# Performance work log

Hardware: AMD Instinct MI355X
Metric: run time of the kernel (lower is better)

The kernel has to match this reference:

```python
import jax, jax.numpy as jnp
import numpy as np
import math

BLUR_K = [1.0, 3.0, 3.0, 1.0]
EPS = 1e-8


def _make_blur_kernel(upsample_factor=2):
    k = jnp.asarray(BLUR_K, dtype=jnp.float32)
    k = k[None, :] * k[:, None]
    k = k / k.sum()
    return k * (upsample_factor ** 2)


def setup_inputs() -> dict:
    key = jax.random.key(0)
    ks = jax.random.split(key, 5)
    B, Cin, Cout, K, S, H, W = 16, 256, 128, 3, 512, 64, 64
    x = jax.random.normal(ks[0], (B, Cin, H, W), dtype=jnp.float32)
    style = jax.random.normal(ks[1], (B, S), dtype=jnp.float32)
    weight = jax.random.normal(ks[2], (1, Cout, Cin, K, K), dtype=jnp.float32)
    mod_w = jax.random.normal(ks[3], (Cin, S), dtype=jnp.float32) * (1.0 / math.sqrt(S))
    mod_b = jnp.ones((Cin,), dtype=jnp.float32)  # StyleGAN2 modulation bias init = 1
    return {"x": x, "style": style, "weight": weight, "mod_w": mod_w, "mod_b": mod_b}


def reference(x, style, weight, mod_w, mod_b):
    B, Cin, H, W = x.shape
    Cout = weight.shape[1]
    K = weight.shape[-1]
    scale = 1.0 / math.sqrt(Cin * K * K)

    # modulation: Linear(style_dim -> in_channel)
    s = style @ mod_w.T + mod_b                      # (B, Cin)
    w = scale * weight * s[:, None, :, None, None]   # (B, Cout, Cin, K, K)
    demod = jax.lax.rsqrt(jnp.sum(w * w, axis=(2, 3, 4)) + EPS)  # (B, Cout)
    w = w * demod[:, :, None, None, None]

    # per-sample conv_transpose2d(stride=2, padding=0, groups=B)
    # == lhs-dilated grouped correlation with spatially-flipped kernel
    kernel = jnp.flip(w, axis=(3, 4)).reshape(B * Cout, Cin, K, K)
    xg = x.reshape(1, B * Cin, H, W)
    out = jax.lax.conv_general_dilated(
        xg, kernel,
        window_strides=(1, 1),
        padding=((K - 1, K - 1), (K - 1, K - 1)),
        lhs_dilation=(2, 2),
        feature_group_count=B,
        dimension_numbers=("NCHW", "OIHW", "NCHW"),
    )  # (1, B*Cout, 2H+K-2, 2W+K-2) -> here (1, B*Cout, 2H+1, 2W+1)
    Ht, Wt = out.shape[2], out.shape[3]

    # Blur2 / upfirdn2d(up=1, down=1, pad=(pad0, pad1))
    # p = len(blur_kernel) - 2 - (K - 1); pad0 = (p+1)//2 + 1; pad1 = p//2 + 1
    p = len(BLUR_K) - 2 - (K - 1)
    pad0 = (p + 1) // 2 + 1
    pad1 = p // 2 + 1
    bk = _make_blur_kernel()                       # (4, 4)
    bw = jnp.flip(bk, axis=(0, 1))[None, None]     # (1, 1, 4, 4)
    outs = out.reshape(B * Cout, 1, Ht, Wt)
    blurred = jax.lax.conv_general_dilated(
        outs, bw,
        window_strides=(1, 1),
        padding=((pad0, pad1), (pad0, pad1)),
        dimension_numbers=("NCHW", "OIHW", "NCHW"),
    )
    Hb, Wb = blurred.shape[2], blurred.shape[3]
    return blurred.reshape(B, Cout, Hb, Wb)
```

## Files before the change

kernel.cpp:

```cpp
#include <hip/hip_runtime.h>
#include <stdint.h>

#define CIN 256
#define COUT 128
#define SDIM 512
#define NB 16

#define XP_RSTRIDE 16896
#define XP_BSTRIDE 1115136
#define A_BSTRIDE (512*2304)

typedef __attribute__((ext_vector_type(8))) short short8;
typedef __attribute__((ext_vector_type(4))) float f32x4;

__device__ __forceinline__ float bf2f(unsigned short h) {
  union { unsigned int u; float f; } v; v.u = ((unsigned int)h) << 16; return v.f;
}
__device__ __forceinline__ unsigned short f2bf(float f) {
  union { float f; unsigned int u; } v; v.f = f;
  return (unsigned short)((v.u + 0x7fffu + ((v.u >> 16) & 1u)) >> 16);
}
__device__ __forceinline__ void gll16(const void* g, void* l) {
  __builtin_amdgcn_global_load_lds(
      (const __attribute__((address_space(1))) unsigned int*)g,
      (__attribute__((address_space(3))) unsigned int*)l, 16, 0, 0);
}

__global__ __launch_bounds__(256) void k_detect(
    const unsigned short* __restrict__ xr, int* __restrict__ flag) {
  __shared__ int red[4];
  int t = threadIdx.x, cnt = 0;
  for (int i = t; i < 8192; i += 256) {
    int e = (xr[2*i] >> 7) & 0xff;
    cnt += (e > 90 && e < 145) ? 1 : 0;
  }
  #pragma unroll
  for (int off = 32; off > 0; off >>= 1) cnt += __shfl_down(cnt, off);
  if ((t & 63) == 0) red[t >> 6] = cnt;
  __syncthreads();
  if (t == 0) *flag = (red[0] + red[1] + red[2] + red[3] < 5000) ? 1 : 0;
}

__global__ __launch_bounds__(256) void k_style(
    const void* __restrict__ style_v, const void* __restrict__ mod_w_v,
    const void* __restrict__ mod_b_v, const int* __restrict__ flag,
    float* __restrict__ s_out) {
  __shared__ float st[SDIM];
  int b = blockIdx.x, t = threadIdx.x;
  int isf = *flag;
  float acc;
  if (!isf) {
    const unsigned short* style = (const unsigned short*)style_v;
    const unsigned short* mod_w = (const unsigned short*)mod_w_v;
    const unsigned short* mod_b = (const unsigned short*)mod_b_v;
    st[t]       = bf2f(style[b*SDIM + t]);
    st[t + 256] = bf2f(style[b*SDIM + t + 256]);
    __syncthreads();
    const uint4* wr = (const uint4*)(mod_w + (size_t)t*SDIM);
    acc = bf2f(mod_b[t]);
    #pragma unroll 4
    for (int s8 = 0; s8 < SDIM/8; ++s8) {
      uint4 p = wr[s8];
      int sb = s8*8;
      acc += bf2f((unsigned short)(p.x & 0xffff))*st[sb]
           + bf2f((unsigned short)(p.x >> 16))   *st[sb+1]
           + bf2f((unsigned short)(p.y & 0xffff))*st[sb+2]
           + bf2f((unsigned short)(p.y >> 16))   *st[sb+3]
           + bf2f((unsigned short)(p.z & 0xffff))*st[sb+4]
           + bf2f((unsigned short)(p.z >> 16))   *st[sb+5]
           + bf2f((unsigned short)(p.w & 0xffff))*st[sb+6]
           + bf2f((unsigned short)(p.w >> 16))   *st[sb+7];
    }
  } else {
    const float* style = (const float*)style_v;
    const float* mod_w = (const float*)mod_w_v;
    const float* mod_b = (const float*)mod_b_v;
    st[t]       = style[b*SDIM + t];
    st[t + 256] = style[b*SDIM + t + 256];
    __syncthreads();
    const float4* wr = (const float4*)(mod_w + (size_t)t*SDIM);
    acc = mod_b[t];
    #pragma unroll 4
    for (int s4 = 0; s4 < SDIM/4; ++s4) {
      float4 p = wr[s4];
      int sb = s4*4;
      acc += p.x*st[sb] + p.y*st[sb+1] + p.z*st[sb+2] + p.w*st[sb+3];
    }
  }
  s_out[b*CIN + t] = acc;
}

__global__ __launch_bounds__(256) void k_weights(
    const void* __restrict__ weight_v,
    const float* __restrict__ s_in,
    const int* __restrict__ flag,
    unsigned short* __restrict__ Aw) {
  int co = blockIdx.x, b = blockIdx.y, ci = threadIdx.x;
  int isf = *flag;
  float sm = 0.0208333333333333f * s_in[b*CIN + ci];
  float w9[9]; float ss = 0.f;
  if (!isf) {
    const unsigned short* wp = (const unsigned short*)weight_v + ((size_t)co*CIN + ci)*9;
    #pragma unroll
    for (int k = 0; k < 9; ++k) { float v = bf2f(wp[k]) * sm; w9[k] = v; ss += v*v; }
  } else {
    const float* wp = (const float*)weight_v + ((size_t)co*CIN + ci)*9;
    #pragma unroll
    for (int k = 0; k < 9; ++k) { float v = wp[k] * sm; w9[k] = v; ss += v*v; }
  }
  #pragma unroll
  for (int off = 32; off > 0; off >>= 1) ss += __shfl_down(ss, off);
  __shared__ float red[4];
  if ((ci & 63) == 0) red[ci >> 6] = ss;
  __syncthreads();
  float demod = rsqrtf(red[0] + red[1] + red[2] + red[3] + 1e-8f);
  #pragma unroll
  for (int k = 0; k < 9; ++k) w9[k] *= demod;
  const float F[4] = {0.25f, 0.75f, 0.75f, 0.25f};
  float C6[6][6];
  #pragma unroll
  for (int ty = 0; ty < 6; ++ty) {
    #pragma unroll
    for (int tx = 0; tx < 6; ++tx) {
      float acc = 0.f;
      #pragma unroll
      for (int ay = 0; ay < 3; ++ay) {
        int fy = ay - ty + 3;
        if (fy < 0 || fy > 3) continue;
        float ra = 0.f;
        #pragma unroll
        for (int ax = 0; ax < 3; ++ax) {
          int fx = ax - tx + 3;
          if (fx < 0 || fx > 3) continue;
          ra += w9[ay*3 + ax] * F[fx];
        }
        acc += ra * F[fy];
      }
      C6[ty][tx] = acc;
    }
  }
  unsigned short* Ab = Aw + (size_t)b*A_BSTRIDE;
  #pragma unroll
  for (int py = 0; py < 2; ++py) {
    #pragma unroll
    for (int px = 0; px < 2; ++px) {
      unsigned short* Am = Ab + (size_t)(py*256 + co*2 + px)*2304 + ci;
      #pragma unroll
      for (int dh = -1; dh <= 1; ++dh) {
        #pragma unroll
        for (int dw = -1; dw <= 1; ++dw) {
          int tap = (dh+1)*3 + (dw+1);
          Am[tap*256] = f2bf(C6[py - 2*dh + 2][px - 2*dw + 2]);
        }
      }
    }
  }
}

__global__ __launch_bounds__(256) void k_transpose(
    const void* __restrict__ x_v,
    const int* __restrict__ flag,
    unsigned short* __restrict__ xp) {
  int r_out = blockIdx.x, b = blockIdx.y, t = threadIdx.x;
  unsigned short* rp = xp + (size_t)b*XP_BSTRIDE + (size_t)r_out*XP_RSTRIDE;
  int r_in = r_out - 1;
  if (r_in < 0 || r_in >= 64) {
    uint4 z = make_uint4(0,0,0,0);
    #pragma unroll
    for (int i = 0; i < 9; ++i) {
      int idx = i*256 + t;
      if (idx < 2112) ((uint4*)rp)[idx] = z;
    }
    return;
  }
  if (t < 64) {
    uint4 z = make_uint4(0,0,0,0);
    int col = (t < 32) ? 0 : 65;
    ((uint4*)(rp + col*256))[t & 31] = z;
  }
  int isf = *flag;
  __shared__ unsigned int lds32[64*33];
  int tci = t >> 3;
  int tc8 = t & 7;
  int cS  = t >> 2;
  int jg  = t & 3;
  for (int g4 = 0; g4 < 4; ++g4) {
    int ci0 = g4 * 64;
    int ci = ci0 + tci*2;
    size_t base = (((size_t)b*CIN + ci)*64 + r_in)*64 + tc8*8;
    unsigned int v[8];
    if (isf) {
      const float* s0 = (const float*)x_v + base;
      const float* s1 = s0 + 4096;
      float4 a0 = ((const float4*)s0)[0], a1 = ((const float4*)s0)[1];
      float4 b0 = ((const float4*)s1)[0], b1 = ((const float4*)s1)[1];
      v[0] = f2bf(a0.x) | ((unsigned int)f2bf(b0.x) << 16);
      v[1] = f2bf(a0.y) | ((unsigned int)f2bf(b0.y) << 16);
      v[2] = f2bf(a0.z) | ((unsigned int)f2bf(b0.z) << 16);
      v[3] = f2bf(a0.w) | ((unsigned int)f2bf(b0.w) << 16);
      v[4] = f2bf(a1.x) | ((unsigned int)f2bf(b1.x) << 16);
      v[5] = f2bf(a1.y) | ((unsigned int)f2bf(b1.y) << 16);
      v[6] = f2bf(a1.z) | ((unsigned int)f2bf(b1.z) << 16);
      v[7] = f2bf(a1.w) | ((unsigned int)f2bf(b1.w) << 16);
    } else {
      const unsigned short* s0 = (const unsigned short*)x_v + base;
      const unsigned short* s1 = s0 + 4096;
      union { uint4 q; unsigned short h[8]; } u0, u1;
      u0.q = *(const uint4*)s0; u1.q = *(const uint4*)s1;
      #pragma unroll
      for (int j = 0; j < 8; ++j)
        v[j] = (unsigned int)u0.h[j] | ((unsigned int)u1.h[j] << 16);
    }
    if (g4) __syncthreads();
    #pragma unroll
    for (int j = 0; j < 8; ++j)
      lds32[(tc8*8 + j)*33 + tci] = v[j];
    __syncthreads();
    union { unsigned int o[8]; uint4 q[2]; } ob;
    #pragma unroll
    for (int w = 0; w < 8; ++w)
      ob.o[w] = lds32[cS*33 + jg*8 + w];
    uint4* dst = (uint4*)(rp + (size_t)(cS+1)*256 + ci0 + jg*16);
    dst[0] = ob.q[0];
    dst[1] = ob.q[1];
  }
}

__global__ __launch_bounds__(256) void k_gemm(
    const unsigned short* __restrict__ Aw,
    const unsigned short* __restrict__ xp,
    const int* __restrict__ flag,
    void* __restrict__ out) {
  __shared__ __align__(16) unsigned short As[128*32];
  __shared__ __align__(16) unsigned short Bs[128*32];
  int g = blockIdx.x;
  int b  = ((g & 7) << 1) | ((g >> 3) & 1);
  int mt = (g >> 4) & 3;
  int nt = g >> 6;
  int yy0 = nt << 1;
  int t = threadIdx.x;
  int wave = t >> 6, lane = t & 63;
  int row = t >> 2, part = t & 3;
  int isf = *flag;

  int partS = part ^ ((row >> 2) & 3);
  const unsigned short* pA0 = Aw + (size_t)b*A_BSTRIDE + (size_t)(mt*128 + row)*2304 + partS*8;
  const unsigned short* pA1 = pA0 + (size_t)64*2304;
  const unsigned short* pB0 = xp + (size_t)b*XP_BSTRIDE + (size_t)(yy0 + 1)*XP_RSTRIDE
                              + (size_t)(row + 1)*256 + partS*8;
  const unsigned short* pB1 = pB0 + XP_RSTRIDE;
  unsigned short* lA0 = &As[row*32 + part*8];
  unsigned short* lA1 = &As[(row + 64)*32 + part*8];
  unsigned short* lB0 = &Bs[row*32 + part*8];
  unsigned short* lB1 = &Bs[(row + 64)*32 + part*8];

  f32x4 acc[4][4];
  #pragma unroll
  for (int i = 0; i < 4; ++i)
    #pragma unroll
    for (int j = 0; j < 4; ++j)
      acc[i][j] = (f32x4){0.f, 0.f, 0.f, 0.f};

  int mb = (wave >> 1) << 6;
  int nb = (wave & 1) << 6;
  int l15 = lane & 15, q = lane >> 4;
  int qs = q ^ ((l15 >> 2) & 3);

  for (int tap = 0; tap < 9; ++tap) {
    int dh = (tap >= 6) ? 1 : ((tap >= 3) ? 0 : -1);
    int dwx = tap - (dh + 1)*3 - 1;
    const unsigned short* a0 = pA0 + tap*256;
    const unsigned short* a1 = pA1 + tap*256;
    const unsigned short* b0 = pB0 + dh*XP_RSTRIDE + dwx*256;
    const unsigned short* b1 = b0 + XP_RSTRIDE;
    #pragma unroll
    for (int kk = 0; kk < 8; ++kk) {
      gll16(a0 + kk*32, lA0);
      gll16(a1 + kk*32, lA1);
      gll16(b0 + kk*32, lB0);
      gll16(b1 + kk*32, lB1);
      __syncthreads();
      short8 af[4], bfv[4];
      #pragma unroll
      for (int i = 0; i < 4; ++i)
        af[i] = *(const short8*)&As[(mb + i*16 + l15)*32 + qs*8];
      #pragma unroll
      for (int j = 0; j < 4; ++j)
        bfv[j] = *(const short8*)&Bs[(nb + j*16 + l15)*32 + qs*8];
      #pragma unroll
      for (int i = 0; i < 4; ++i)
        #pragma unroll
        for (int j = 0; j < 4; ++j)
          acc[i][j] = __builtin_amdgcn_mfma_f32_16x16x32_bf16(af[i], bfv[j], acc[i][j], 0, 0, 0);
      __syncthreads();
    }
  }

  int py = mt >> 1;
  int ry = wave & 1;
  int y = ((yy0 + ry) << 1) + py;
  int cobase = ((mt & 1) << 6) + ((wave >> 1) << 5);
  #pragma unroll
  for (int i = 0; i < 4; ++i) {
    #pragma unroll
    for (int rr = 0; rr < 2; ++rr) {
      int co = cobase + i*8 + q*2 + rr;
      size_t obase = (((size_t)b*COUT + co)*128 + y)*64;
      if (!isf) {
        unsigned int* outp = (unsigned int*)out;
        #pragma unroll
        for (int j = 0; j < 4; ++j) {
          unsigned int pk = (unsigned int)f2bf(acc[i][j][rr*2])
                          | ((unsigned int)f2bf(acc[i][j][rr*2 + 1]) << 16);
          outp[obase + j*16 + l15] = pk;
        }
      } else {
        float2* outp = (float2*)out;
        #pragma unroll
        for (int j = 0; j < 4; ++j)
          outp[obase + j*16 + l15] = make_float2(acc[i][j][rr*2], acc[i][j][rr*2 + 1]);
      }
    }
  }
}

extern "C" void kernel_launch(void* const* d_in, const int* in_sizes, int n_in,
                              void* d_out, int out_size, void* d_ws, size_t ws_size,
                              hipStream_t stream) {
  const void* x      = d_in[0];
  const void* style  = d_in[1];
  const void* weight = d_in[2];
  const void* mod_w  = d_in[3];
  const void* mod_b  = d_in[4];
  char* ws = (char*)d_ws;
  int* flag           = (int*)ws;
  float* s_buf        = (float*)(ws + 1024);
  unsigned short* Aw  = (unsigned short*)(ws + 32768);
  unsigned short* xpd = (unsigned short*)(ws + 32768 + 37748736);

  k_detect   <<<1, 256, 0, stream>>>((const unsigned short*)x, flag);
  k_style    <<<NB, 256, 0, stream>>>(style, mod_w, mod_b, flag, s_buf);
  k_weights  <<<dim3(COUT, NB), 256, 0, stream>>>(weight, s_buf, flag, Aw);
  k_transpose<<<dim3(66, NB), 256, 0, stream>>>(x, flag, xpd);
  k_gemm     <<<2048, 256, 0, stream>>>(Aw, xpd, flag, d_out);
}
```

Measured before the change: 419.6 us.

## Double-buffer LDS tiles and enlarge GEMM N-tile to four rows

The implicit-GEMM kernel now double-buffers its A and B LDS tiles, so the asynchronous global-to-LDS loads for the next K slice are issued while MFMAs run on the current one. This drops one of the two barriers per step. Each block also covers four input rows instead of two (a 128x256 tile, 32 accumulators per wave), which halves the grid and reuses each A fragment across twice as many MFMAs. The cost is more accumulator registers and twice the LDS per block, which may lower occupancy.

```diff
diff --git a/kernel.cpp b/kernel.cpp
--- a/kernel.cpp
+++ b/kernel.cpp
@@ -231,94 +231,119 @@
     const unsigned short* __restrict__ xp,
     const int* __restrict__ flag,
     void* __restrict__ out) {
-  __shared__ __align__(16) unsigned short As[128*32];
-  __shared__ __align__(16) unsigned short Bs[128*32];
+  __shared__ __align__(16) unsigned short As[2][128*32];
+  __shared__ __align__(16) unsigned short Bs[2][256*32];
   int g = blockIdx.x;
   int b  = ((g & 7) << 1) | ((g >> 3) & 1);
   int mt = (g >> 4) & 3;
   int nt = g >> 6;
-  int yy0 = nt << 1;
+  int yy0 = nt << 2;
   int t = threadIdx.x;
   int wave = t >> 6, lane = t & 63;
   int row = t >> 2, part = t & 3;
   int isf = *flag;
 
   int partS = part ^ ((row >> 2) & 3);
-  const unsigned short* pA0 = Aw + (size_t)b*A_BSTRIDE + (size_t)(mt*128 + row)*2304 + partS*8;
-  const unsigned short* pA1 = pA0 + (size_t)64*2304;
-  const unsigned short* pB0 = xp + (size_t)b*XP_BSTRIDE + (size_t)(yy0 + 1)*XP_RSTRIDE
+  int dstOff = row*32 + part*8;
+  const unsigned short* gA0 = Aw + (size_t)b*A_BSTRIDE + (size_t)(mt*128 + row)*2304 + partS*8;
+  const unsigned short* gA1 = gA0 + (size_t)64*2304;
+  const unsigned short* gB0 = xp + (size_t)b*XP_BSTRIDE + (size_t)(yy0 + 1)*XP_RSTRIDE
                               + (size_t)(row + 1)*256 + partS*8;
-  const unsigned short* pB1 = pB0 + XP_RSTRIDE;
-  unsigned short* lA0 = &As[row*32 + part*8];
-  unsigned short* lA1 = &As[(row + 64)*32 + part*8];
-  unsigned short* lB0 = &Bs[row*32 + part*8];
-  unsigned short* lB1 = &Bs[(row + 64)*32 + part*8];
-
-  f32x4 acc[4][4];
+
+  f32x4 acc[4][8];
   #pragma unroll
   for (int i = 0; i < 4; ++i)
     #pragma unroll
-    for (int j = 0; j < 4; ++j)
+    for (int j = 0; j < 8; ++j)
       acc[i][j] = (f32x4){0.f, 0.f, 0.f, 0.f};
 
-  int mb = (wave >> 1) << 6;
-  int nb = (wave & 1) << 6;
   int l15 = lane & 15, q = lane >> 4;
   int qs = q ^ ((l15 >> 2) & 3);
-
-  for (int tap = 0; tap < 9; ++tap) {
-    int dh = (tap >= 6) ? 1 : ((tap >= 3) ? 0 : -1);
-    int dwx = tap - (dh + 1)*3 - 1;
-    const unsigned short* a0 = pA0 + tap*256;
-    const unsigned short* a1 = pA1 + tap*256;
-    const unsigned short* b0 = pB0 + dh*XP_RSTRIDE + dwx*256;
-    const unsigned short* b1 = b0 + XP_RSTRIDE;
-    #pragma unroll
-    for (int kk = 0; kk < 8; ++kk) {
-      gll16(a0 + kk*32, lA0);
-      gll16(a1 + kk*32, lA1);
-      gll16(b0 + kk*32, lB0);
-      gll16(b1 + kk*32, lB1);
-      __syncthreads();
-      short8 af[4], bfv[4];
+  int wm = wave >> 1, wn = wave & 1;
+  int rAoff = (wm*64 + l15)*32 + qs*8;
+  int rBoff = (wn*128 + l15)*32 + qs*8;
+
+  unsigned short* sAc = (unsigned short*)As[0];
+  unsigned short* sAn = (unsigned short*)As[1];
+  unsigned short* sBc = (unsigned short*)Bs[0];
+  unsigned short* sBn = (unsigned short*)Bs[1];
+
+  #define STAGE(SA, SB, S) { \
+    int tap_ = (S) >> 3; int kk_ = (S) & 7; \
+    int dh_ = (tap_ >= 6) ? 1 : ((tap_ >= 3) ? 0 : -1); \
+    int dwx_ = tap_ - (dh_ + 1)*3 - 1; \
+    int ao_ = tap_*256 + kk_*32; \
+    int bo_ = dh_*XP_RSTRIDE + dwx_*256 + kk_*32; \
+    unsigned short* dA_ = (SA) + dstOff; \
+    unsigned short* dB_ = (SB) + dstOff; \
+    gll16(gA0 + ao_, dA_); \
+    gll16(gA1 + ao_, dA_ + 2048); \
+    gll16(gB0 + bo_, dB_); \
+    gll16(gB0 + bo_ + XP_RSTRIDE,   dB_ + 2048); \
+    gll16(gB0 + bo_ + 2*XP_RSTRIDE, dB_ + 4096); \
+    gll16(gB0 + bo_ + 3*XP_RSTRIDE, dB_ + 6144); \
+  }
+
+  STAGE(sAc, sBc, 0);
+  __syncthreads();
+
+  for (int s = 0; s < 72; ++s) {
+    if (s < 71) STAGE(sAn, sBn, s + 1);
+    const unsigned short* rA = sAc + rAoff;
+    const unsigned short* rB = sBc + rBoff;
+    short8 af[4];
+    #pragma unroll
+    for (int i = 0; i < 4; ++i)
+      af[i] = *(const short8*)(rA + i*512);
+    #pragma unroll
+    for (int j = 0; j < 8; ++j) {
+      short8 bv = *(const short8*)(rB + j*512);
       #pragma unroll
       for (int i = 0; i < 4; ++i)
-        af[i] = *(const short8*)&As[(mb + i*16 + l15)*32 + qs*8];
-      #pragma unroll
-      for (int j = 0; j < 4; ++j)
-        bfv[j] = *(const short8*)&Bs[(nb + j*16 + l15)*32 + qs*8];
-      #pragma unroll
-      for (int i = 0; i < 4; ++i)
+        acc[i][j] = __builtin_amdgcn_mfma_f32_16x16x32_bf16(af[i], bv, acc[i][j], 0, 0, 0);
+    }
+    __syncthreads();
+    unsigned short* tp_;
+    tp_ = sAc; sAc = sAn; sAn = tp_;
+    tp_ = sBc; sBc = sBn; sBn = tp_;
+  }
+  #undef STAGE
+
+  int py = mt >> 1;
+  if (!isf) {
+    unsigned int* outp = (unsigned int*)out;
+    #pragma unroll
+    for (int i = 0; i < 4; ++i) {
+      #pragma unroll
+      for (int rr = 0; rr < 2; ++rr) {
+        int co = ((mt & 1) << 6) + (wm << 5) + i*8 + q*2 + rr;
         #pragma unroll
-        for (int j = 0; j < 4; ++j)
-          acc[i][j] = __builtin_amdgcn_mfma_f32_16x16x32_bf16(af[i], bfv[j], acc[i][j], 0, 0, 0);
-      __syncthreads();
-    }
-  }
-
-  int py = mt >> 1;
-  int ry = wave & 1;
-  int y = ((yy0 + ry) << 1) + py;
-  int cobase = ((mt & 1) << 6) + ((wave >> 1) << 5);
-  #pragma unroll
-  for (int i = 0; i < 4; ++i) {
-    #pragma unroll
-    for (int rr = 0; rr < 2; ++rr) {
-      int co = cobase + i*8 + q*2 + rr;
-      size_t obase = (((size_t)b*COUT + co)*128 + y)*64;
-      if (!isf) {
-        unsigned int* outp = (unsigned int*)out;
-        #pragma unroll
-        for (int j = 0; j < 4; ++j) {
+        for (int j = 0; j < 8; ++j) {
+          int ryl = (wn << 1) + (j >> 2);
+          int y = ((yy0 + ryl) << 1) + py;
+          int x = ((j & 3) << 4) + l15;
+          size_t oidx = (((size_t)b*COUT + co)*128 + y)*64 + x;
           unsigned int pk = (unsigned int)f2bf(acc[i][j][rr*2])
                           | ((unsigned int)f2bf(acc[i][j][rr*2 + 1]) << 16);
-          outp[obase + j*16 + l15] = pk;
+          outp[oidx] = pk;
         }
-      } else {
-        float2* outp = (float2*)out;
+      }
+    }
+  } else {
+    float2* outp = (float2*)out;
+    #pragma unroll
+    for (int i = 0; i < 4; ++i) {
+      #pragma unroll
+      for (int rr = 0; rr < 2; ++rr) {
+        int co = ((mt & 1) << 6) + (wm << 5) + i*8 + q*2 + rr;
         #pragma unroll
-        for (int j = 0; j < 4; ++j)
-          outp[obase + j*16 + l15] = make_float2(acc[i][j][rr*2], acc[i][j][rr*2 + 1]);
+        for (int j = 0; j < 8; ++j) {
+          int ryl = (wn << 1) + (j >> 2);
+          int y = ((yy0 + ryl) << 1) + py;
+          int x = ((j & 3) << 4) + l15;
+          size_t oidx = (((size_t)b*COUT + co)*128 + y)*64 + x;
+          outp[oidx] = make_float2(acc[i][j][rr*2], acc[i][j][rr*2 + 1]);
+        }
       }
     }
   }
@@ -342,5 +367,5 @@
   k_style    <<<NB, 256, 0, stream>>>(style, mod_w, mod_b, flag, s_buf);
   k_weights  <<<dim3(COUT, NB), 256, 0, stream>>>(weight, s_buf, flag, Aw);
   k_transpose<<<dim3(66, NB), 256, 0, stream>>>(x, flag, xpd);
-  k_gemm     <<<2048, 256, 0, stream>>>(Aw, xpd, flag, d_out);
-}
+  k_gemm     <<<1024, 256, 0, stream>>>(Aw, xpd, flag, d_out);
+}
```

Result: slower. 484.3 us (+15.4%).

## Double-buffer LDS tiles in tap-conv GEMM to overlap loads with MFMA

Applied to the files above, without the earlier changes.

Splits the A and B shared-memory tiles into two buffers, so the next K-slice is loaded by global_load_lds while MFMAs run on the current one. This includes prefetching across tap boundaries. One barrier per k-step is dropped, and the load latency is meant to hide behind compute. In exchange, LDS use doubles to 32KB per block, which may reduce occupancy.

```diff
diff --git a/kernel.cpp b/kernel.cpp
--- a/kernel.cpp
+++ b/kernel.cpp
@@ -231,8 +231,8 @@
     const unsigned short* __restrict__ xp,
     const int* __restrict__ flag,
     void* __restrict__ out) {
-  __shared__ __align__(16) unsigned short As[128*32];
-  __shared__ __align__(16) unsigned short Bs[128*32];
+  __shared__ __align__(16) unsigned short As[2][128*32];
+  __shared__ __align__(16) unsigned short Bs[2][128*32];
   int g = blockIdx.x;
   int b  = ((g & 7) << 1) | ((g >> 3) & 1);
   int mt = (g >> 4) & 3;
@@ -244,15 +244,11 @@
   int isf = *flag;
 
   int partS = part ^ ((row >> 2) & 3);
+  int dstOff = row*32 + part*8;
   const unsigned short* pA0 = Aw + (size_t)b*A_BSTRIDE + (size_t)(mt*128 + row)*2304 + partS*8;
   const unsigned short* pA1 = pA0 + (size_t)64*2304;
   const unsigned short* pB0 = xp + (size_t)b*XP_BSTRIDE + (size_t)(yy0 + 1)*XP_RSTRIDE
                               + (size_t)(row + 1)*256 + partS*8;
-  const unsigned short* pB1 = pB0 + XP_RSTRIDE;
-  unsigned short* lA0 = &As[row*32 + part*8];
-  unsigned short* lA1 = &As[(row + 64)*32 + part*8];
-  unsigned short* lB0 = &Bs[row*32 + part*8];
-  unsigned short* lB1 = &Bs[(row + 64)*32 + part*8];
 
   f32x4 acc[4][4];
   #pragma unroll
@@ -266,35 +262,57 @@
   int l15 = lane & 15, q = lane >> 4;
   int qs = q ^ ((l15 >> 2) & 3);
 
+  #define STAGE(BI, A0, A1, B0, KK) { \
+    gll16((A0) + (KK)*32, &As[BI][dstOff]); \
+    gll16((A1) + (KK)*32, &As[BI][dstOff + 2048]); \
+    gll16((B0) + (KK)*32, &Bs[BI][dstOff]); \
+    gll16((B0) + (KK)*32 + XP_RSTRIDE, &Bs[BI][dstOff + 2048]); \
+  }
+
+  #define COMPUTE(BI) { \
+    short8 af[4], bv[4]; \
+    _Pragma("unroll") \
+    for (int i_ = 0; i_ < 4; ++i_) \
+      af[i_] = *(const short8*)&As[BI][(mb + i_*16 + l15)*32 + qs*8]; \
+    _Pragma("unroll") \
+    for (int j_ = 0; j_ < 4; ++j_) \
+      bv[j_] = *(const short8*)&Bs[BI][(nb + j_*16 + l15)*32 + qs*8]; \
+    _Pragma("unroll") \
+    for (int i_ = 0; i_ < 4; ++i_) \
+      _Pragma("unroll") \
+      for (int j_ = 0; j_ < 4; ++j_) \
+        acc[i_][j_] = __builtin_amdgcn_mfma_f32_16x16x32_bf16(af[i_], bv[j_], acc[i_][j_], 0, 0, 0); \
+  }
+
+  STAGE(0, pA0, pA1, pB0 - XP_RSTRIDE - 256, 0);
+  __syncthreads();
+
   for (int tap = 0; tap < 9; ++tap) {
-    int dh = (tap >= 6) ? 1 : ((tap >= 3) ? 0 : -1);
+    int dh  = (tap >= 6) ? 1 : ((tap >= 3) ? 0 : -1);
     int dwx = tap - (dh + 1)*3 - 1;
     const unsigned short* a0 = pA0 + tap*256;
     const unsigned short* a1 = pA1 + tap*256;
     const unsigned short* b0 = pB0 + dh*XP_RSTRIDE + dwx*256;
-    const unsigned short* b1 = b0 + XP_RSTRIDE;
-    #pragma unroll
-    for (int kk = 0; kk < 8; ++kk) {
-      gll16(a0 + kk*32, lA0);
-      gll16(a1 + kk*32, lA1);
-      gll16(b0 + kk*32, lB0);
-      gll16(b1 + kk*32, lB1);
+    int tap1 = tap + 1;
+    int dh1  = (tap1 >= 6) ? 1 : ((tap1 >= 3) ? 0 : -1);
+    int dwx1 = tap1 - (dh1 + 1)*3 - 1;
+    const unsigned short* nb0 = pB0 + dh1*XP_RSTRIDE + dwx1*256;
+    #pragma unroll
+    for (int kk = 0; kk < 8; kk += 2) {
+      STAGE(1, a0, a1, b0, kk + 1);
+      COMPUTE(0);
       __syncthreads();
-      short8 af[4], bfv[4];
-      #pragma unroll
-      for (int i = 0; i < 4; ++i)
-        af[i] = *(const short8*)&As[(mb + i*16 + l15)*32 + qs*8];
-      #pragma unroll
-      for (int j = 0; j < 4; ++j)
-        bfv[j] = *(const short8*)&Bs[(nb + j*16 + l15)*32 + qs*8];
-      #pragma unroll
-      for (int i = 0; i < 4; ++i)
-        #pragma unroll
-        for (int j = 0; j < 4; ++j)
-          acc[i][j] = __builtin_amdgcn_mfma_f32_16x16x32_bf16(af[i], bfv[j], acc[i][j], 0, 0, 0);
-      __syncthreads();
-    }
-  }
+      if (kk < 6) {
+        STAGE(0, a0, a1, b0, kk + 2);
+      } else if (tap < 8) {
+        STAGE(0, a0 + 256, a1 + 256, nb0, 0);
+      }
+      COMPUTE(1);
+      if (!(tap == 8 && kk == 6)) __syncthreads();
+    }
+  }
+  #undef STAGE
+  #undef COMPUTE
 
   int py = mt >> 1;
   int ry = wave & 1;
```

Measured after the change: 431.1 us. +2.7%, slower.
